# Kernel optimization log

Measured on AMD Instinct MI355X. Metric: run time of the kernel, lower is better.

Reference implementation:

```python
import jax, jax.numpy as jnp
import numpy as np

N = 1_000_000
D1 = 16          # n_input_1 (first-layer features, cols 0:16)
D2 = 16          # n_input_2 (second-layer features, cols 16:32)
NC = 64          # n_clusters (first layer)
NCPC = 8         # n_clusters_per_cluster (second layer)


def setup_inputs() -> dict:
    key = jax.random.key(0)
    k1, k2, k3 = jax.random.split(key, 3)
    x = jax.random.normal(k1, (N, D1 + D2), dtype=jnp.float32)
    centers_outer = jax.random.normal(k2, (NC, D1), dtype=jnp.float32)
    centers_inner = jax.random.normal(k3, (NC, NCPC, D2), dtype=jnp.float32)
    return {"x": x, "centers_outer": centers_outer, "centers_inner": centers_inner}


def reference(x, centers_outer, centers_inner):
    # x: [N, D1+D2]; input_1_idx = cols [0:D1], input_2_idx = cols [D1:D1+D2]
    x1 = x[:, :D1]
    x2 = x[:, D1:]

    # First-layer nearest-centroid assignment (squared Euclidean).
    # ||x1 - c||^2 = ||x1||^2 - 2 x1.c + ||c||^2; the ||x1||^2 term is
    # constant over clusters so it does not affect the argmin.
    d1 = jnp.sum(centers_outer ** 2, axis=-1)[None, :] - 2.0 * (x1 @ centers_outer.T)  # [N, NC]
    outer = jnp.argmin(d1, axis=1)  # [N] int

    # Second-layer assignment: each sample only compares against the NCPC
    # sub-centers of its outer cluster (this fuses the original per-cluster
    # torch.where gather/scatter loop into one vectorized pass).
    sub = centers_inner[outer]  # [N, NCPC, D2] gather
    d2 = jnp.sum(sub ** 2, axis=-1) - 2.0 * jnp.einsum("nd,nkd->nk", x2, sub)  # [N, NCPC]
    inner = jnp.argmin(d2, axis=1)  # [N]

    return inner + outer * NCPC  # combined cluster id in [0, NC*NCPC)
```

## Files before the change

kernel.cpp:

```cpp
#include <hip/hip_runtime.h>

constexpr int D = 16;
constexpr int NC = 64;
constexpr int NCPC = 8;
constexpr int OSTRIDE = NCPC * D + 4;
constexpr int BLOCK = 256;
constexpr int NPT = 4;

typedef __attribute__((ext_vector_type(8)))  short short8;
typedef __attribute__((ext_vector_type(16))) float f32x16;

static __device__ __forceinline__ unsigned f2bf(float f) {
    unsigned u = __float_as_uint(f);
    u += 0x7FFFu + ((u >> 16) & 1u);
    return u >> 16;
}
static __device__ __forceinline__ float bf2f(unsigned h) {
    return __uint_as_float(h << 16);
}

__global__ __launch_bounds__(BLOCK, 4)
void cluster_kernel(const float* __restrict__ x,
                    const float* __restrict__ co,
                    const float* __restrict__ ci,
                    int* __restrict__ out, int n)
{
    __shared__ __align__(16) float s_ci[NC * OSTRIDE];
    __shared__ float s_inorm[NC * 9];

    const int t    = threadIdx.x;
    const int lane = t & 63;
    const int wave = t >> 6;

    const float4* ci4 = (const float4*)ci;
    #pragma unroll
    for (int i = 0; i < 8; ++i) {
        int idx = t + i * BLOCK;
        int o = idx >> 5, f = idx & 31;
        float4 v = ci4[idx];
        *(float4*)&s_ci[o * OSTRIDE + f * 4] = v;
    }
    #pragma unroll
    for (int ii = 0; ii < 2; ++ii) {
        int i = t + ii * BLOCK;
        const float* src = ci + i * D;
        float s = 0.f;
        #pragma unroll
        for (int k = 0; k < D; ++k) s = fmaf(src[k], src[k], s);
        s_inorm[(i >> 3) * 9 + (i & 7)] = s;
    }

    float my_norm;
    {
        const float* c = co + lane * D;
        float s = 0.f;
        #pragma unroll
        for (int k = 0; k < D; ++k) s = fmaf(c[k], c[k], s);
        my_norm = s;
    }

    const int hi  = lane >> 5;
    const int ks  = hi * 8;
    const int hi4 = hi * 4;

    float n_init[2][16];
    #pragma unroll
    for (int tc = 0; tc < 2; ++tc) {
        #pragma unroll
        for (int r = 0; r < 16; ++r) {
            int c = tc * 32 + (r & 3) + 8 * (r >> 2) + hi4;
            n_init[tc][r] = __int_as_float(
                __builtin_amdgcn_ds_bpermute(c << 2, __float_as_int(my_norm)));
        }
    }

    short8 a_h[2], a_m[2], a_l[2];
    #pragma unroll
    for (int tc = 0; tc < 2; ++tc) {
        const float* cp = co + (tc * 32 + (lane & 31)) * D + ks;
        float4 v0 = *(const float4*)cp;
        float4 v1 = *(const float4*)(cp + 4);
        float vv[8] = {v0.x,v0.y,v0.z,v0.w, v1.x,v1.y,v1.z,v1.w};
        #pragma unroll
        for (int j = 0; j < 8; ++j) {
            float v = vv[j];
            unsigned h = f2bf(v); float r1 = v - bf2f(h);
            unsigned m = f2bf(r1); r1 = r1 - bf2f(m);
            unsigned l2 = f2bf(r1);
            a_h[tc][j] = (short)h; a_m[tc][j] = (short)m; a_l[tc][j] = (short)l2;
        }
    }
    __syncthreads();

    const int blockStart = blockIdx.x * (BLOCK * NPT);
    #pragma unroll 1
    for (int it = 0; it < NPT; ++it) {
        const int S = blockStart + it * BLOCK + wave * 64;

        int bo0 = 0, bo1 = 0;
        #pragma unroll
        for (int pt = 0; pt < 2; ++pt) {
            int P = S + pt * 32 + (lane & 31);
            P = P < n ? P : n - 1;
            const float* xp = x + (size_t)P * 32 + ks;
            float4 w0 = *(const float4*)xp;
            float4 w1 = *(const float4*)(xp + 4);
            float vv[8] = {w0.x,w0.y,w0.z,w0.w, w1.x,w1.y,w1.z,w1.w};
            short8 b_h, b_m, b_l;
            #pragma unroll
            for (int j = 0; j < 8; ++j) {
                float v = -2.0f * vv[j];
                unsigned h = f2bf(v); float r1 = v - bf2f(h);
                unsigned m = f2bf(r1); r1 = r1 - bf2f(m);
                unsigned l2 = f2bf(r1);
                b_h[j] = (short)h; b_m[j] = (short)m; b_l[j] = (short)l2;
            }

            f32x16 acc0, acc1;
            #pragma unroll
            for (int r = 0; r < 16; ++r) { acc0[r] = n_init[0][r]; acc1[r] = n_init[1][r]; }
            acc0 = __builtin_amdgcn_mfma_f32_32x32x16_bf16(a_h[0], b_h, acc0, 0,0,0);
            acc0 = __builtin_amdgcn_mfma_f32_32x32x16_bf16(a_h[0], b_m, acc0, 0,0,0);
            acc0 = __builtin_amdgcn_mfma_f32_32x32x16_bf16(a_m[0], b_h, acc0, 0,0,0);
            acc0 = __builtin_amdgcn_mfma_f32_32x32x16_bf16(a_h[0], b_l, acc0, 0,0,0);
            acc0 = __builtin_amdgcn_mfma_f32_32x32x16_bf16(a_m[0], b_m, acc0, 0,0,0);
            acc0 = __builtin_amdgcn_mfma_f32_32x32x16_bf16(a_l[0], b_h, acc0, 0,0,0);
            acc1 = __builtin_amdgcn_mfma_f32_32x32x16_bf16(a_h[1], b_h, acc1, 0,0,0);
            acc1 = __builtin_amdgcn_mfma_f32_32x32x16_bf16(a_h[1], b_m, acc1, 0,0,0);
            acc1 = __builtin_amdgcn_mfma_f32_32x32x16_bf16(a_m[1], b_h, acc1, 0,0,0);
            acc1 = __builtin_amdgcn_mfma_f32_32x32x16_bf16(a_h[1], b_l, acc1, 0,0,0);
            acc1 = __builtin_amdgcn_mfma_f32_32x32x16_bf16(a_m[1], b_m, acc1, 0,0,0);
            acc1 = __builtin_amdgcn_mfma_f32_32x32x16_bf16(a_l[1], b_h, acc1, 0,0,0);

            float bestd = 3.4e38f; int bc = 0;
            #pragma unroll
            for (int tc = 0; tc < 2; ++tc) {
                #pragma unroll
                for (int r = 0; r < 16; ++r) {
                    float d  = tc ? acc1[r] : acc0[r];
                    int  cb = tc * 32 + (r & 3) + 8 * (r >> 2);
                    if (d < bestd) { bestd = d; bc = cb; }
                }
            }
            int bestc = bc + hi4;
            int pidx = (lane ^ 32) << 2;
            float od = __int_as_float(
                __builtin_amdgcn_ds_bpermute(pidx, __float_as_int(bestd)));
            int   oc = __builtin_amdgcn_ds_bpermute(pidx, bestc);
            if (od < bestd || (od == bestd && oc < bestc)) { bestd = od; bestc = oc; }
            if (pt == 0) bo0 = bestc; else bo1 = bestc;
        }
        const int bo = (lane < 32) ? bo0 : bo1;

        const int p = S + lane;
        const int q = p < n ? p : n - 1;
        const float4* yp = (const float4*)(x + (size_t)q * 32 + 16);
        float4 ya = yp[0], yb = yp[1], yc = yp[2], yd = yp[3];
        float x2[16] = {ya.x,ya.y,ya.z,ya.w, yb.x,yb.y,yb.z,yb.w,
                        yc.x,yc.y,yc.z,yc.w, yd.x,yd.y,yd.z,yd.w};
        const float* cbp = s_ci + bo * OSTRIDE;
        const float* nb  = s_inorm + bo * 9;
        float bestd2 = 3.4e38f;
        int bk = 0;
        #pragma unroll
        for (int k = 0; k < NCPC; ++k) {
            float4 e0 = *(const float4*)&cbp[k * D + 0];
            float4 e1 = *(const float4*)&cbp[k * D + 4];
            float4 e2 = *(const float4*)&cbp[k * D + 8];
            float4 e3 = *(const float4*)&cbp[k * D + 12];
            float dot = 0.f;
            dot = fmaf(x2[0],  e0.x, dot); dot = fmaf(x2[1],  e0.y, dot);
            dot = fmaf(x2[2],  e0.z, dot); dot = fmaf(x2[3],  e0.w, dot);
            dot = fmaf(x2[4],  e1.x, dot); dot = fmaf(x2[5],  e1.y, dot);
            dot = fmaf(x2[6],  e1.z, dot); dot = fmaf(x2[7],  e1.w, dot);
            dot = fmaf(x2[8],  e2.x, dot); dot = fmaf(x2[9],  e2.y, dot);
            dot = fmaf(x2[10], e2.z, dot); dot = fmaf(x2[11], e2.w, dot);
            dot = fmaf(x2[12], e3.x, dot); dot = fmaf(x2[13], e3.y, dot);
            dot = fmaf(x2[14], e3.z, dot); dot = fmaf(x2[15], e3.w, dot);
            float d2v = fmaf(-2.f, dot, nb[k]);
            if (d2v < bestd2) { bestd2 = d2v; bk = k; }
        }

        if (p < n) out[p] = bo * NCPC + bk;
    }
}

extern "C" void kernel_launch(void* const* d_in, const int* in_sizes, int n_in,
                              void* d_out, int out_size, void* d_ws, size_t ws_size,
                              hipStream_t stream) {
    const float* x  = (const float*)d_in[0];
    const float* co = (const float*)d_in[1];
    const float* ci = (const float*)d_in[2];
    int* out = (int*)d_out;
    int n = in_sizes[0] / 32;
    int blocks = (n + BLOCK * NPT - 1) / (BLOCK * NPT);
    cluster_kernel<<<blocks, BLOCK, 0, stream>>>(x, co, ci, out, n);
}
```

Before: 191.9 us.

## Split fused clustering kernel into separate outer and inner kernels

Splits the single fused kernel into two launches. The first computes the outer-cluster assignment with MFMA and writes one byte per sample to workspace. The second loads the inner centers into shared memory once per 512-thread block and does the per-sample inner argmin. The intent is to drop the large shared-memory footprint and its sync from the MFMA kernel so occupancy rises, at the cost of an extra launch, an extra pass that re-reads the x2 half of the input, and a byte-array round-trip through memory.

```diff
diff --git a/kernel.cpp b/kernel.cpp
--- a/kernel.cpp
+++ b/kernel.cpp
@@ -4,8 +4,10 @@
 constexpr int NC = 64;
 constexpr int NCPC = 8;
 constexpr int OSTRIDE = NCPC * D + 4;
-constexpr int BLOCK = 256;
-constexpr int NPT = 4;
+constexpr int BLOCK1 = 256;
+constexpr int NPT1   = 4;
+constexpr int BLOCK2 = 512;
+constexpr int NPT2   = 4;
 
 typedef __attribute__((ext_vector_type(8)))  short short8;
 typedef __attribute__((ext_vector_type(16))) float f32x16;
@@ -19,36 +21,14 @@
     return __uint_as_float(h << 16);
 }
 
-__global__ __launch_bounds__(BLOCK, 4)
-void cluster_kernel(const float* __restrict__ x,
-                    const float* __restrict__ co,
-                    const float* __restrict__ ci,
-                    int* __restrict__ out, int n)
+__global__ __launch_bounds__(BLOCK1, 4)
+void outer_kernel(const float* __restrict__ x,
+                  const float* __restrict__ co,
+                  unsigned char* __restrict__ bo_out, int n)
 {
-    __shared__ __align__(16) float s_ci[NC * OSTRIDE];
-    __shared__ float s_inorm[NC * 9];
-
     const int t    = threadIdx.x;
     const int lane = t & 63;
     const int wave = t >> 6;
-
-    const float4* ci4 = (const float4*)ci;
-    #pragma unroll
-    for (int i = 0; i < 8; ++i) {
-        int idx = t + i * BLOCK;
-        int o = idx >> 5, f = idx & 31;
-        float4 v = ci4[idx];
-        *(float4*)&s_ci[o * OSTRIDE + f * 4] = v;
-    }
-    #pragma unroll
-    for (int ii = 0; ii < 2; ++ii) {
-        int i = t + ii * BLOCK;
-        const float* src = ci + i * D;
-        float s = 0.f;
-        #pragma unroll
-        for (int k = 0; k < D; ++k) s = fmaf(src[k], src[k], s);
-        s_inorm[(i >> 3) * 9 + (i & 7)] = s;
-    }
 
     float my_norm;
     {
@@ -90,12 +70,11 @@
             a_h[tc][j] = (short)h; a_m[tc][j] = (short)m; a_l[tc][j] = (short)l2;
         }
     }
-    __syncthreads();
-
-    const int blockStart = blockIdx.x * (BLOCK * NPT);
+
+    const int blockStart = blockIdx.x * (BLOCK1 * NPT1);
     #pragma unroll 1
-    for (int it = 0; it < NPT; ++it) {
-        const int S = blockStart + it * BLOCK + wave * 64;
+    for (int it = 0; it < NPT1; ++it) {
+        const int S = blockStart + it * BLOCK1 + wave * 64;
 
         int bo0 = 0, bo1 = 0;
         #pragma unroll
@@ -137,7 +116,7 @@
             for (int tc = 0; tc < 2; ++tc) {
                 #pragma unroll
                 for (int r = 0; r < 16; ++r) {
-                    float d  = tc ? acc1[r] : acc0[r];
+                    float d = tc ? acc1[r] : acc0[r];
                     int  cb = tc * 32 + (r & 3) + 8 * (r >> 2);
                     if (d < bestd) { bestd = d; bc = cb; }
                 }
@@ -150,38 +129,74 @@
             if (od < bestd || (od == bestd && oc < bestc)) { bestd = od; bestc = oc; }
             if (pt == 0) bo0 = bestc; else bo1 = bestc;
         }
-        const int bo = (lane < 32) ? bo0 : bo1;
-
         const int p = S + lane;
-        const int q = p < n ? p : n - 1;
-        const float4* yp = (const float4*)(x + (size_t)q * 32 + 16);
-        float4 ya = yp[0], yb = yp[1], yc = yp[2], yd = yp[3];
-        float x2[16] = {ya.x,ya.y,ya.z,ya.w, yb.x,yb.y,yb.z,yb.w,
-                        yc.x,yc.y,yc.z,yc.w, yd.x,yd.y,yd.z,yd.w};
-        const float* cbp = s_ci + bo * OSTRIDE;
-        const float* nb  = s_inorm + bo * 9;
-        float bestd2 = 3.4e38f;
-        int bk = 0;
-        #pragma unroll
-        for (int k = 0; k < NCPC; ++k) {
-            float4 e0 = *(const float4*)&cbp[k * D + 0];
-            float4 e1 = *(const float4*)&cbp[k * D + 4];
-            float4 e2 = *(const float4*)&cbp[k * D + 8];
-            float4 e3 = *(const float4*)&cbp[k * D + 12];
-            float dot = 0.f;
-            dot = fmaf(x2[0],  e0.x, dot); dot = fmaf(x2[1],  e0.y, dot);
-            dot = fmaf(x2[2],  e0.z, dot); dot = fmaf(x2[3],  e0.w, dot);
-            dot = fmaf(x2[4],  e1.x, dot); dot = fmaf(x2[5],  e1.y, dot);
-            dot = fmaf(x2[6],  e1.z, dot); dot = fmaf(x2[7],  e1.w, dot);
-            dot = fmaf(x2[8],  e2.x, dot); dot = fmaf(x2[9],  e2.y, dot);
-            dot = fmaf(x2[10], e2.z, dot); dot = fmaf(x2[11], e2.w, dot);
-            dot = fmaf(x2[12], e3.x, dot); dot = fmaf(x2[13], e3.y, dot);
-            dot = fmaf(x2[14], e3.z, dot); dot = fmaf(x2[15], e3.w, dot);
-            float d2v = fmaf(-2.f, dot, nb[k]);
-            if (d2v < bestd2) { bestd2 = d2v; bk = k; }
-        }
-
-        if (p < n) out[p] = bo * NCPC + bk;
+        if (p < n) bo_out[p] = (unsigned char)((lane < 32) ? bo0 : bo1);
+    }
+}
+
+__global__ __launch_bounds__(BLOCK2, 4)
+void inner_kernel(const float* __restrict__ x,
+                  const float* __restrict__ ci,
+                  const unsigned char* __restrict__ bo_in,
+                  int* __restrict__ out, int n)
+{
+    __shared__ __align__(16) float s_ci[NC * OSTRIDE];
+    __shared__ float s_inorm[NC * 9];
+
+    const int t = threadIdx.x;
+
+    const float4* ci4 = (const float4*)ci;
+    #pragma unroll
+    for (int i = 0; i < 4; ++i) {
+        int idx = t + i * BLOCK2;
+        int o = idx >> 5, f = idx & 31;
+        float4 v = ci4[idx];
+        *(float4*)&s_ci[o * OSTRIDE + f * 4] = v;
+    }
+    {
+        int i = t;
+        const float* src = ci + i * D;
+        float s = 0.f;
+        #pragma unroll
+        for (int k = 0; k < D; ++k) s = fmaf(src[k], src[k], s);
+        s_inorm[(i >> 3) * 9 + (i & 7)] = s;
+    }
+    __syncthreads();
+
+    const int base = blockIdx.x * (BLOCK2 * NPT2) + t;
+    #pragma unroll 1
+    for (int it = 0; it < NPT2; ++it) {
+        int p = base + it * BLOCK2;
+        if (p < n) {
+            const int bo = bo_in[p];
+            const float4* yp = (const float4*)(x + (size_t)p * 32 + 16);
+            float4 ya = yp[0], yb = yp[1], yc = yp[2], yd = yp[3];
+            float x2[16] = {ya.x,ya.y,ya.z,ya.w, yb.x,yb.y,yb.z,yb.w,
+                            yc.x,yc.y,yc.z,yc.w, yd.x,yd.y,yd.z,yd.w};
+            const float* cb = s_ci + bo * OSTRIDE;
+            const float* nb = s_inorm + bo * 9;
+            float bestd2 = 3.4e38f;
+            int bk = 0;
+            #pragma unroll
+            for (int k = 0; k < NCPC; ++k) {
+                float4 e0 = *(const float4*)&cb[k * D + 0];
+                float4 e1 = *(const float4*)&cb[k * D + 4];
+                float4 e2 = *(const float4*)&cb[k * D + 8];
+                float4 e3 = *(const float4*)&cb[k * D + 12];
+                float dot = 0.f;
+                dot = fmaf(x2[0],  e0.x, dot); dot = fmaf(x2[1],  e0.y, dot);
+                dot = fmaf(x2[2],  e0.z, dot); dot = fmaf(x2[3],  e0.w, dot);
+                dot = fmaf(x2[4],  e1.x, dot); dot = fmaf(x2[5],  e1.y, dot);
+                dot = fmaf(x2[6],  e1.z, dot); dot = fmaf(x2[7],  e1.w, dot);
+                dot = fmaf(x2[8],  e2.x, dot); dot = fmaf(x2[9],  e2.y, dot);
+                dot = fmaf(x2[10], e2.z, dot); dot = fmaf(x2[11], e2.w, dot);
+                dot = fmaf(x2[12], e3.x, dot); dot = fmaf(x2[13], e3.y, dot);
+                dot = fmaf(x2[14], e3.z, dot); dot = fmaf(x2[15], e3.w, dot);
+                float d2v = fmaf(-2.f, dot, nb[k]);
+                if (d2v < bestd2) { bestd2 = d2v; bk = k; }
+            }
+            out[p] = bo * NCPC + bk;
+        }
     }
 }
 
@@ -193,6 +208,10 @@
     const float* ci = (const float*)d_in[2];
     int* out = (int*)d_out;
     int n = in_sizes[0] / 32;
-    int blocks = (n + BLOCK * NPT - 1) / (BLOCK * NPT);
-    cluster_kernel<<<blocks, BLOCK, 0, stream>>>(x, co, ci, out, n);
-}
+    unsigned char* bo_ws = (unsigned char*)d_ws;
+
+    int blocks1 = (n + BLOCK1 * NPT1 - 1) / (BLOCK1 * NPT1);
+    outer_kernel<<<blocks1, BLOCK1, 0, stream>>>(x, co, bo_ws, n);
+    int blocks2 = (n + BLOCK2 * NPT2 - 1) / (BLOCK2 * NPT2);
+    inner_kernel<<<blocks2, BLOCK2, 0, stream>>>(x, ci, bo_ws, out, n);
+}
```

New measurement: 208.7 us. 8.8% more time.

## Halve points per block, prefetch next tile, keep outer norms in shared memory

Applied to the files above, without the earlier changes.

Points per block drop from four tiles to two, and the rolled loop becomes two explicitly unrolled stages. The first-layer x loads for the second tile are issued before the first tile's MFMA work, so global latency can overlap compute. Outer-centroid norms now sit in shared memory and are read per scan instead of being held in 32 registers via bpermute, which cuts register pressure. The cost is twice as many blocks, so the shared-memory centroid staging is repeated twice as often.

```diff
diff --git a/kernel.cpp b/kernel.cpp
--- a/kernel.cpp
+++ b/kernel.cpp
@@ -5,7 +5,7 @@
 constexpr int NCPC = 8;
 constexpr int OSTRIDE = NCPC * D + 4;
 constexpr int BLOCK = 256;
-constexpr int NPT = 4;
+constexpr int NPT = 2;
 
 typedef __attribute__((ext_vector_type(8)))  short short8;
 typedef __attribute__((ext_vector_type(16))) float f32x16;
@@ -17,6 +17,83 @@
 }
 static __device__ __forceinline__ float bf2f(unsigned h) {
     return __uint_as_float(h << 16);
+}
+
+static __device__ __forceinline__ void conv_pt(float4 w0, float4 w1,
+                                               short8* bh, short8* bm, short8* bl) {
+    float vv[8] = {w0.x,w0.y,w0.z,w0.w, w1.x,w1.y,w1.z,w1.w};
+    #pragma unroll
+    for (int j = 0; j < 8; ++j) {
+        float v = -2.0f * vv[j];
+        unsigned h = f2bf(v); float r1 = v - bf2f(h);
+        unsigned m = f2bf(r1); r1 = r1 - bf2f(m);
+        unsigned l2 = f2bf(r1);
+        (*bh)[j] = (short)h; (*bm)[j] = (short)m; (*bl)[j] = (short)l2;
+    }
+}
+
+static __device__ __forceinline__ int mfma_scan(const short8* a_h, const short8* a_m,
+                                                const short8* a_l,
+                                                short8 bh, short8 bm, short8 bl,
+                                                const float* s_onorm, int hi4) {
+    float bestd = 3.4e38f; int bc = 0;
+    #pragma unroll
+    for (int tc = 0; tc < 2; ++tc) {
+        f32x16 acc;
+        #pragma unroll
+        for (int g = 0; g < 4; ++g) {
+            float4 nn = *(const float4*)&s_onorm[tc * 32 + g * 8 + hi4];
+            acc[g*4+0] = nn.x; acc[g*4+1] = nn.y; acc[g*4+2] = nn.z; acc[g*4+3] = nn.w;
+        }
+        acc = __builtin_amdgcn_mfma_f32_32x32x16_bf16(a_h[tc], bh, acc, 0,0,0);
+        acc = __builtin_amdgcn_mfma_f32_32x32x16_bf16(a_h[tc], bm, acc, 0,0,0);
+        acc = __builtin_amdgcn_mfma_f32_32x32x16_bf16(a_m[tc], bh, acc, 0,0,0);
+        acc = __builtin_amdgcn_mfma_f32_32x32x16_bf16(a_h[tc], bl, acc, 0,0,0);
+        acc = __builtin_amdgcn_mfma_f32_32x32x16_bf16(a_m[tc], bm, acc, 0,0,0);
+        acc = __builtin_amdgcn_mfma_f32_32x32x16_bf16(a_l[tc], bh, acc, 0,0,0);
+        #pragma unroll
+        for (int r = 0; r < 16; ++r) {
+            float d = acc[r];
+            int  c = tc * 32 + (r & 3) + 8 * (r >> 2);
+            if (d < bestd) { bestd = d; bc = c; }
+        }
+    }
+    int bestc = bc + hi4;
+    int lane = (int)(threadIdx.x & 63);
+    int pidx = (lane ^ 32) << 2;
+    float od = __int_as_float(
+        __builtin_amdgcn_ds_bpermute(pidx, __float_as_int(bestd)));
+    int   oc = __builtin_amdgcn_ds_bpermute(pidx, bestc);
+    if (od < bestd || (od == bestd && oc < bestc)) bestc = oc;
+    return bestc;
+}
+
+static __device__ __forceinline__ int inner_argmin(const float* s_ci,
+                                                   const float* s_inorm,
+                                                   int bo, const float* x2) {
+    const float* cb = s_ci + bo * OSTRIDE;
+    const float* nb = s_inorm + bo * 9;
+    float bestd2 = 3.4e38f;
+    int bk = 0;
+    #pragma unroll
+    for (int k = 0; k < NCPC; ++k) {
+        float4 e0 = *(const float4*)&cb[k * D + 0];
+        float4 e1 = *(const float4*)&cb[k * D + 4];
+        float4 e2 = *(const float4*)&cb[k * D + 8];
+        float4 e3 = *(const float4*)&cb[k * D + 12];
+        float dot = 0.f;
+        dot = fmaf(x2[0],  e0.x, dot); dot = fmaf(x2[1],  e0.y, dot);
+        dot = fmaf(x2[2],  e0.z, dot); dot = fmaf(x2[3],  e0.w, dot);
+        dot = fmaf(x2[4],  e1.x, dot); dot = fmaf(x2[5],  e1.y, dot);
+        dot = fmaf(x2[6],  e1.z, dot); dot = fmaf(x2[7],  e1.w, dot);
+        dot = fmaf(x2[8],  e2.x, dot); dot = fmaf(x2[9],  e2.y, dot);
+        dot = fmaf(x2[10], e2.z, dot); dot = fmaf(x2[11], e2.w, dot);
+        dot = fmaf(x2[12], e3.x, dot); dot = fmaf(x2[13], e3.y, dot);
+        dot = fmaf(x2[14], e3.z, dot); dot = fmaf(x2[15], e3.w, dot);
+        float d2v = fmaf(-2.f, dot, nb[k]);
+        if (d2v < bestd2) { bestd2 = d2v; bk = k; }
+    }
+    return bk;
 }
 
 __global__ __launch_bounds__(BLOCK, 4)
@@ -26,6 +103,7 @@
                     int* __restrict__ out, int n)
 {
     __shared__ __align__(16) float s_ci[NC * OSTRIDE];
+    __shared__ __align__(16) float s_onorm[NC];
     __shared__ float s_inorm[NC * 9];
 
     const int t    = threadIdx.x;
@@ -49,30 +127,17 @@
         for (int k = 0; k < D; ++k) s = fmaf(src[k], src[k], s);
         s_inorm[(i >> 3) * 9 + (i & 7)] = s;
     }
-
-    float my_norm;
-    {
-        const float* c = co + lane * D;
+    if (t < NC) {
+        const float* c = co + t * D;
         float s = 0.f;
         #pragma unroll
         for (int k = 0; k < D; ++k) s = fmaf(c[k], c[k], s);
-        my_norm = s;
+        s_onorm[t] = s;
     }
 
     const int hi  = lane >> 5;
     const int ks  = hi * 8;
     const int hi4 = hi * 4;
-
-    float n_init[2][16];
-    #pragma unroll
-    for (int tc = 0; tc < 2; ++tc) {
-        #pragma unroll
-        for (int r = 0; r < 16; ++r) {
-            int c = tc * 32 + (r & 3) + 8 * (r >> 2) + hi4;
-            n_init[tc][r] = __int_as_float(
-                __builtin_amdgcn_ds_bpermute(c << 2, __float_as_int(my_norm)));
-        }
-    }
 
     short8 a_h[2], a_m[2], a_l[2];
     #pragma unroll
@@ -92,95 +157,62 @@
     }
     __syncthreads();
 
-    const int blockStart = blockIdx.x * (BLOCK * NPT);
-    #pragma unroll 1
-    for (int it = 0; it < NPT; ++it) {
-        const int S = blockStart + it * BLOCK + wave * 64;
-
-        int bo0 = 0, bo1 = 0;
-        #pragma unroll
-        for (int pt = 0; pt < 2; ++pt) {
-            int P = S + pt * 32 + (lane & 31);
-            P = P < n ? P : n - 1;
-            const float* xp = x + (size_t)P * 32 + ks;
-            float4 w0 = *(const float4*)xp;
-            float4 w1 = *(const float4*)(xp + 4);
-            float vv[8] = {w0.x,w0.y,w0.z,w0.w, w1.x,w1.y,w1.z,w1.w};
-            short8 b_h, b_m, b_l;
-            #pragma unroll
-            for (int j = 0; j < 8; ++j) {
-                float v = -2.0f * vv[j];
-                unsigned h = f2bf(v); float r1 = v - bf2f(h);
-                unsigned m = f2bf(r1); r1 = r1 - bf2f(m);
-                unsigned l2 = f2bf(r1);
-                b_h[j] = (short)h; b_m[j] = (short)m; b_l[j] = (short)l2;
-            }
-
-            f32x16 acc0, acc1;
-            #pragma unroll
-            for (int r = 0; r < 16; ++r) { acc0[r] = n_init[0][r]; acc1[r] = n_init[1][r]; }
-            acc0 = __builtin_amdgcn_mfma_f32_32x32x16_bf16(a_h[0], b_h, acc0, 0,0,0);
-            acc0 = __builtin_amdgcn_mfma_f32_32x32x16_bf16(a_h[0], b_m, acc0, 0,0,0);
-            acc0 = __builtin_amdgcn_mfma_f32_32x32x16_bf16(a_m[0], b_h, acc0, 0,0,0);
-            acc0 = __builtin_amdgcn_mfma_f32_32x32x16_bf16(a_h[0], b_l, acc0, 0,0,0);
-            acc0 = __builtin_amdgcn_mfma_f32_32x32x16_bf16(a_m[0], b_m, acc0, 0,0,0);
-            acc0 = __builtin_amdgcn_mfma_f32_32x32x16_bf16(a_l[0], b_h, acc0, 0,0,0);
-            acc1 = __builtin_amdgcn_mfma_f32_32x32x16_bf16(a_h[1], b_h, acc1, 0,0,0);
-            acc1 = __builtin_amdgcn_mfma_f32_32x32x16_bf16(a_h[1], b_m, acc1, 0,0,0);
-            acc1 = __builtin_amdgcn_mfma_f32_32x32x16_bf16(a_m[1], b_h, acc1, 0,0,0);
-            acc1 = __builtin_amdgcn_mfma_f32_32x32x16_bf16(a_h[1], b_l, acc1, 0,0,0);
-            acc1 = __builtin_amdgcn_mfma_f32_32x32x16_bf16(a_m[1], b_m, acc1, 0,0,0);
-            acc1 = __builtin_amdgcn_mfma_f32_32x32x16_bf16(a_l[1], b_h, acc1, 0,0,0);
-
-            float bestd = 3.4e38f; int bc = 0;
-            #pragma unroll
-            for (int tc = 0; tc < 2; ++tc) {
-                #pragma unroll
-                for (int r = 0; r < 16; ++r) {
-                    float d  = tc ? acc1[r] : acc0[r];
-                    int  cb = tc * 32 + (r & 3) + 8 * (r >> 2);
-                    if (d < bestd) { bestd = d; bc = cb; }
-                }
-            }
-            int bestc = bc + hi4;
-            int pidx = (lane ^ 32) << 2;
-            float od = __int_as_float(
-                __builtin_amdgcn_ds_bpermute(pidx, __float_as_int(bestd)));
-            int   oc = __builtin_amdgcn_ds_bpermute(pidx, bestc);
-            if (od < bestd || (od == bestd && oc < bestc)) { bestd = od; bestc = oc; }
-            if (pt == 0) bo0 = bestc; else bo1 = bestc;
-        }
-        const int bo = (lane < 32) ? bo0 : bo1;
-
-        const int p = S + lane;
+    const int S0 = blockIdx.x * (BLOCK * NPT) + wave * 64;
+    const int S1 = S0 + BLOCK;
+    const int l31 = lane & 31;
+
+    int P00 = S0 + l31;        P00 = P00 < n ? P00 : n - 1;
+    int P01 = S0 + 32 + l31;   P01 = P01 < n ? P01 : n - 1;
+    const float* a0p = x + (size_t)P00 * 32 + ks;
+    const float* a1p = x + (size_t)P01 * 32 + ks;
+    float4 c00 = *(const float4*)a0p, c01 = *(const float4*)(a0p + 4);
+    float4 c10 = *(const float4*)a1p, c11 = *(const float4*)(a1p + 4);
+
+    {
+        const int p = S0 + lane;
         const int q = p < n ? p : n - 1;
         const float4* yp = (const float4*)(x + (size_t)q * 32 + 16);
         float4 ya = yp[0], yb = yp[1], yc = yp[2], yd = yp[3];
+
+        short8 bh0, bm0, bl0, bh1, bm1, bl1;
+        conv_pt(c00, c01, &bh0, &bm0, &bl0);
+        conv_pt(c10, c11, &bh1, &bm1, &bl1);
+
+        int Q0 = S1 + l31;        Q0 = Q0 < n ? Q0 : n - 1;
+        int Q1 = S1 + 32 + l31;   Q1 = Q1 < n ? Q1 : n - 1;
+        const float* b0p = x + (size_t)Q0 * 32 + ks;
+        const float* b1p = x + (size_t)Q1 * 32 + ks;
+        float4 n00 = *(const float4*)b0p, n01 = *(const float4*)(b0p + 4);
+        float4 n10 = *(const float4*)b1p, n11 = *(const float4*)(b1p + 4);
+
+        int bo0 = mfma_scan(a_h, a_m, a_l, bh0, bm0, bl0, s_onorm, hi4);
+        int bo1 = mfma_scan(a_h, a_m, a_l, bh1, bm1, bl1, s_onorm, hi4);
+        int bo  = (lane < 32) ? bo0 : bo1;
+
         float x2[16] = {ya.x,ya.y,ya.z,ya.w, yb.x,yb.y,yb.z,yb.w,
                         yc.x,yc.y,yc.z,yc.w, yd.x,yd.y,yd.z,yd.w};
-        const float* cbp = s_ci + bo * OSTRIDE;
-        const float* nb  = s_inorm + bo * 9;
-        float bestd2 = 3.4e38f;
-        int bk = 0;
-        #pragma unroll
-        for (int k = 0; k < NCPC; ++k) {
-            float4 e0 = *(const float4*)&cbp[k * D + 0];
-            float4 e1 = *(const float4*)&cbp[k * D + 4];
-            float4 e2 = *(const float4*)&cbp[k * D + 8];
-            float4 e3 = *(const float4*)&cbp[k * D + 12];
-            float dot = 0.f;
-            dot = fmaf(x2[0],  e0.x, dot); dot = fmaf(x2[1],  e0.y, dot);
-            dot = fmaf(x2[2],  e0.z, dot); dot = fmaf(x2[3],  e0.w, dot);
-            dot = fmaf(x2[4],  e1.x, dot); dot = fmaf(x2[5],  e1.y, dot);
-            dot = fmaf(x2[6],  e1.z, dot); dot = fmaf(x2[7],  e1.w, dot);
-            dot = fmaf(x2[8],  e2.x, dot); dot = fmaf(x2[9],  e2.y, dot);
-            dot = fmaf(x2[10], e2.z, dot); dot = fmaf(x2[11], e2.w, dot);
-            dot = fmaf(x2[12], e3.x, dot); dot = fmaf(x2[13], e3.y, dot);
-            dot = fmaf(x2[14], e3.z, dot); dot = fmaf(x2[15], e3.w, dot);
-            float d2v = fmaf(-2.f, dot, nb[k]);
-            if (d2v < bestd2) { bestd2 = d2v; bk = k; }
-        }
-
+        int bk = inner_argmin(s_ci, s_inorm, bo, x2);
+        if (p < n) out[p] = bo * NCPC + bk;
+
+        c00 = n00; c01 = n01; c10 = n10; c11 = n11;
+    }
+    {
+        const int p = S1 + lane;
+        const int q = p < n ? p : n - 1;
+        const float4* yp = (const float4*)(x + (size_t)q * 32 + 16);
+        float4 ya = yp[0], yb = yp[1], yc = yp[2], yd = yp[3];
+
+        short8 bh0, bm0, bl0, bh1, bm1, bl1;
+        conv_pt(c00, c01, &bh0, &bm0, &bl0);
+        conv_pt(c10, c11, &bh1, &bm1, &bl1);
+
+        int bo0 = mfma_scan(a_h, a_m, a_l, bh0, bm0, bl0, s_onorm, hi4);
+        int bo1 = mfma_scan(a_h, a_m, a_l, bh1, bm1, bl1, s_onorm, hi4);
+        int bo  = (lane < 32) ? bo0 : bo1;
+
+        float x2[16] = {ya.x,ya.y,ya.z,ya.w, yb.x,yb.y,yb.z,yb.w,
+                        yc.x,yc.y,yc.z,yc.w, yd.x,yd.y,yd.z,yd.w};
+        int bk = inner_argmin(s_ci, s_inorm, bo, x2);
         if (p < n) out[p] = bo * NCPC + bk;
     }
 }
```

Result: no change. 192.4 us (+0.3%).
